# Optimization experiments

Hardware: AMD Instinct MI355X
Metric: run time of the kernel (lower is better)

Reference implementation:

```python
import jax, jax.numpy as jnp
import numpy as np

N_NODES = 50000

def setup_inputs() -> dict:
    key = jax.random.key(0)
    ks = jax.random.split(key, 6)
    x = jax.random.normal(ks[0], (N_NODES, 64), dtype=jnp.float32)
    src = jax.random.randint(ks[1], (800000,), 0, N_NODES, dtype=jnp.int64)
    dst = jax.random.randint(ks[2], (800000,), 0, N_NODES, dtype=jnp.int64)
    W = jax.random.normal(ks[3], (64, 64), dtype=jnp.float32) * (1.0 / np.sqrt(64))
    b = jnp.zeros((64,), dtype=jnp.float32)
    Wr = jax.random.normal(ks[4], (64, 64), dtype=jnp.float32) * (1.0 / np.sqrt(64))
    br = jnp.zeros((64,), dtype=jnp.float32)
    return {"x": x, "src": src, "dst": dst, "W": W, "b": b, "Wr": Wr, "br": br}


def reference(x, src, dst, W, b, Wr, br):
    # DGL GraphConv, norm='both', allow_zero_in_degree=True:
    #   h = D_in^{-1/2} * (A^T (D_out^{-1/2} * x)) @ W + b, degrees clamped to >=1
    n = x.shape[0]
    ones = jnp.ones(src.shape[0], dtype=x.dtype)
    out_deg = jax.ops.segment_sum(ones, src, num_segments=n)  # out-degree of each node
    in_deg = jax.ops.segment_sum(ones, dst, num_segments=n)   # in-degree of each node
    norm_src = jax.lax.rsqrt(jnp.clip(out_deg, 1.0, None))[:, None]  # [N,1]
    norm_dst = jax.lax.rsqrt(jnp.clip(in_deg, 1.0, None))[:, None]   # [N,1]
    x_src = x * norm_src
    # SpMM aggregate: sum messages from src to dst
    agg = jax.ops.segment_sum(x_src[src], dst, num_segments=n)  # [N, in_dim]
    agg = agg * norm_dst
    h = agg @ W + b
    res = x @ Wr + br
    return h + res
```

## Files before the change

### kernel.cpp

```cpp
#include <hip/hip_runtime.h>


#define TILE 4096

typedef __attribute__((ext_vector_type(4))) _Float16 half4;

__global__ __launch_bounds__(256) void bucket_hist_kernel(
    const int* __restrict__ src, const int* __restrict__ dst,
    int* __restrict__ H, int e, int nb) {
    __shared__ int hd[256], hs[256];
    int t = threadIdx.x, blk = blockIdx.x;
    hd[t] = 0; hs[t] = 0;
    __syncthreads();
    int base = blk * TILE;
    #pragma unroll
    for (int s = 0; s < 16; ++s) {
        int j = base + s * 256 + t;
        if (j < e) {
            atomicAdd(&hd[dst[j] >> 8], 1);
            atomicAdd(&hs[src[j] >> 8], 1);
        }
    }
    __syncthreads();
    H[t * nb + blk]            = hd[t];
    H[256 * nb + t * nb + blk] = hs[t];
}

__global__ void partial_kernel(const int* __restrict__ cnt, int* __restrict__ part, int m) {
    __shared__ int sm[256];
    int t = threadIdx.x;
    int base = blockIdx.x * 4096 + t * 16;
    int s = 0;
    if (base + 16 <= m) {
        const int4* p = (const int4*)(cnt + base);
        #pragma unroll
        for (int k = 0; k < 4; ++k) { int4 v = p[k]; s += v.x + v.y + v.z + v.w; }
    } else {
        for (int k = 0; k < 16; ++k) if (base + k < m) s += cnt[base + k];
    }
    sm[t] = s;
    __syncthreads();
    for (int st = 128; st > 0; st >>= 1) {
        if (t < st) sm[t] += sm[t + st];
        __syncthreads();
    }
    if (t == 0) part[blockIdx.x] = sm[0];
}

__global__ void scan_final_kernel(const int* __restrict__ cnt, const int* __restrict__ part,
                                  int* __restrict__ Hoff, int m, int nbs) {
    __shared__ int sm[256], sp[256];
    int t = threadIdx.x;
    int pv = (t < nbs) ? part[t] : 0;
    sp[t] = pv;
    __syncthreads();
    for (int d = 1; d < 256; d <<= 1) {
        int add = (t >= d) ? sp[t - d] : 0;
        __syncthreads();
        sp[t] += add;
        __syncthreads();
    }
    sp[t] -= pv;
    __syncthreads();
    int blkoff = sp[blockIdx.x];

    int base = blockIdx.x * 4096 + t * 16;
    int v[16];
    #pragma unroll
    for (int k = 0; k < 16; ++k) v[k] = (base + k < m) ? cnt[base + k] : 0;
    int s = 0;
    #pragma unroll
    for (int k = 0; k < 16; ++k) { int x = v[k]; v[k] = s; s += x; }
    sm[t] = s;
    __syncthreads();
    for (int d = 1; d < 256; d <<= 1) {
        int add = (t >= d) ? sm[t - d] : 0;
        __syncthreads();
        sm[t] += add;
        __syncthreads();
    }
    int tb = sm[t] - s + blkoff;
    #pragma unroll
    for (int k = 0; k < 16; ++k)
        if (base + k < m) Hoff[base + k] = v[k] + tb;
}

__global__ __launch_bounds__(256) void bucket_scatter_kernel(
    const int* __restrict__ src, const int* __restrict__ dst,
    const int* __restrict__ Hoff,
    int* __restrict__ packed, unsigned char* __restrict__ ksrc2,
    int e, int nb) {
    __shared__ int dcur[256], scur[256];
    int t = threadIdx.x, blk = blockIdx.x;
    dcur[t] = Hoff[t * nb + blk];
    scur[t] = Hoff[256 * nb + t * nb + blk] - e;
    __syncthreads();
    int base = blk * TILE;
    #pragma unroll
    for (int s2 = 0; s2 < 16; ++s2) {
        int j = base + s2 * 256 + t;
        if (j < e) {
            int d = dst[j], sv = src[j];
            int pd = atomicAdd(&dcur[d >> 8], 1);
            packed[pd] = (sv << 8) | (d & 255);
            int ps = atomicAdd(&scur[sv >> 8], 1);
            ksrc2[ps] = (unsigned char)(sv & 255);
        }
    }
}

__global__ __launch_bounds__(256) void csr_outdeg_kernel(
    const int* __restrict__ packed, const unsigned char* __restrict__ ksrc2,
    const int* __restrict__ Hoff,
    int* __restrict__ roff, unsigned short* __restrict__ col,
    const float4* __restrict__ x4, half4* __restrict__ xsh,
    int n, int e, int nb, int nrange) {
    __shared__ int lh[256], sm[256];
    int t = threadIdx.x;
    int r = blockIdx.x;
    if (r < nrange) {
        int beg = Hoff[r * nb];
        int end = (r + 1 < nrange) ? Hoff[(r + 1) * nb] : e;
        lh[t] = 0;
        __syncthreads();
        for (int j = beg + t; j < end; j += 256)
            atomicAdd(&lh[packed[j] & 255], 1);
        __syncthreads();
        int v0 = lh[t];
        sm[t] = v0;
        __syncthreads();
        for (int d = 1; d < 256; d <<= 1) {
            int add = (t >= d) ? sm[t - d] : 0;
            __syncthreads();
            sm[t] += add;
            __syncthreads();
        }
        int excl = sm[t] - v0;
        int v = r * 256 + t;
        if (v < n) roff[v] = beg + excl;
        __syncthreads();
        lh[t] = excl;
        __syncthreads();
        for (int j = beg + t; j < end; j += 256) {
            int p = packed[j];
            int pos = beg + atomicAdd(&lh[p & 255], 1);
            col[pos] = (unsigned short)(p >> 8);
        }
        if (r == 0 && t == 0) roff[n] = e;
    } else {
        r -= nrange;
        lh[t] = 0;
        __syncthreads();
        int beg = Hoff[256 * nb + r * nb] - e;
        int end = (r + 1 < nrange) ? (Hoff[256 * nb + (r + 1) * nb] - e) : e;
        for (int j = beg + t; j < end; j += 256)
            atomicAdd(&lh[ksrc2[j]], 1);
        __syncthreads();
        int base = r * 256;
        for (int i = t; i < 256 * 16; i += 256) {
            int row = i >> 4, g = base + row;
            if (g < n) {
                float s = rsqrtf((float)max(lh[row], 1));
                float4 v = x4[(long)g * 16 + (i & 15)];
                half4 h;
                h.x = (_Float16)(v.x * s);
                h.y = (_Float16)(v.y * s);
                h.z = (_Float16)(v.z * s);
                h.w = (_Float16)(v.w * s);
                xsh[(long)g * 16 + (i & 15)] = h;
            }
        }
    }
}

__global__ __launch_bounds__(256) void gather_kernel(
    const half4* __restrict__ xsh, const unsigned short* __restrict__ col,
    const int* __restrict__ roff,
    float4* __restrict__ agg4, int n) {
    int lane = threadIdx.x & 63;
    int node = (blockIdx.x * 256 + threadIdx.x) >> 6;
    if (node >= n) return;
    node = __builtin_amdgcn_readfirstlane(node);

    int beg = roff[node];
    int end = roff[node + 1];
    int g = lane >> 4;
    int q = lane & 15;

    float4 acc = make_float4(0.f, 0.f, 0.f, 0.f);
    int j = beg;
    for (; j + 16 <= end; j += 16) {
        int s0 = col[j + g];
        int s1 = col[j + 4 + g];
        int s2 = col[j + 8 + g];
        int s3 = col[j + 12 + g];
        half4 v0 = xsh[(long)s0 * 16 + q];
        half4 v1 = xsh[(long)s1 * 16 + q];
        half4 v2 = xsh[(long)s2 * 16 + q];
        half4 v3 = xsh[(long)s3 * 16 + q];
        acc.x += ((float)v0.x + (float)v1.x) + ((float)v2.x + (float)v3.x);
        acc.y += ((float)v0.y + (float)v1.y) + ((float)v2.y + (float)v3.y);
        acc.z += ((float)v0.z + (float)v1.z) + ((float)v2.z + (float)v3.z);
        acc.w += ((float)v0.w + (float)v1.w) + ((float)v2.w + (float)v3.w);
    }
    for (; j + 8 <= end; j += 8) {
        int s0 = col[j + g];
        int s1 = col[j + 4 + g];
        half4 v0 = xsh[(long)s0 * 16 + q];
        half4 v1 = xsh[(long)s1 * 16 + q];
        acc.x += (float)v0.x + (float)v1.x;
        acc.y += (float)v0.y + (float)v1.y;
        acc.z += (float)v0.z + (float)v1.z;
        acc.w += (float)v0.w + (float)v1.w;
    }
    for (; j < end; j += 4) {
        int jj = j + g;
        int s   = (jj < end) ? (int)col[jj] : node;
        float m = (jj < end) ? 1.f : 0.f;
        half4 v = xsh[(long)s * 16 + q];
        acc.x += (float)v.x * m;
        acc.y += (float)v.y * m;
        acc.z += (float)v.z * m;
        acc.w += (float)v.w * m;
    }

    acc.x += __shfl_down(acc.x, 32);
    acc.y += __shfl_down(acc.y, 32);
    acc.z += __shfl_down(acc.z, 32);
    acc.w += __shfl_down(acc.w, 32);
    acc.x += __shfl_down(acc.x, 16);
    acc.y += __shfl_down(acc.y, 16);
    acc.z += __shfl_down(acc.z, 16);
    acc.w += __shfl_down(acc.w, 16);

    float nd = rsqrtf((float)max(end - beg, 1));
    if (lane < 16) {
        acc.x *= nd; acc.y *= nd; acc.z *= nd; acc.w *= nd;
        agg4[(long)node * 16 + q] = acc;
    }
}

#define OR 32
__global__ __launch_bounds__(256) void out_kernel(
    const float4* __restrict__ agg4, const float4* __restrict__ x4,
    const float* __restrict__ W, const float* __restrict__ b,
    const float* __restrict__ Wr, const float* __restrict__ br,
    float* __restrict__ out, int n) {
    __shared__ float4 sA[OR * 16];
    __shared__ float4 sX[OR * 16];
    int t = threadIdx.x;
    int c = t & 63;
    int base = blockIdx.x * OR;

    float4 wA[16], wR[16];
    #pragma unroll
    for (int q = 0; q < 16; ++q) {
        wA[q].x = W[(4 * q + 0) * 64 + c];
        wA[q].y = W[(4 * q + 1) * 64 + c];
        wA[q].z = W[(4 * q + 2) * 64 + c];
        wA[q].w = W[(4 * q + 3) * 64 + c];
        wR[q].x = Wr[(4 * q + 0) * 64 + c];
        wR[q].y = Wr[(4 * q + 1) * 64 + c];
        wR[q].z = Wr[(4 * q + 2) * 64 + c];
        wR[q].w = Wr[(4 * q + 3) * 64 + c];
    }

    #pragma unroll
    for (int i = 0; i < 2; ++i) {
        int qi = t + 256 * i;
        int row = base + (qi >> 4);
        float4 z = make_float4(0.f, 0.f, 0.f, 0.f);
        sA[qi] = (row < n) ? agg4[(long)row * 16 + (qi & 15)] : z;
        sX[qi] = (row < n) ? x4[(long)row * 16 + (qi & 15)] : z;
    }
    __syncthreads();

    int w = t >> 6;
    float bias = b[c] + br[c];
    for (int r = w * 8; r < w * 8 + 8; ++r) {
        float a0 = 0.f, a1 = 0.f, r0 = 0.f, r1 = 0.f;
        #pragma unroll
        for (int q = 0; q < 16; q += 2) {
            float4 av0 = sA[r * 16 + q];
            float4 av1 = sA[r * 16 + q + 1];
            float4 xv0 = sX[r * 16 + q];
            float4 xv1 = sX[r * 16 + q + 1];
            a0 += av0.x * wA[q].x + av0.y * wA[q].y + av0.z * wA[q].z + av0.w * wA[q].w;
            a1 += av1.x * wA[q + 1].x + av1.y * wA[q + 1].y + av1.z * wA[q + 1].z + av1.w * wA[q + 1].w;
            r0 += xv0.x * wR[q].x + xv0.y * wR[q].y + xv0.z * wR[q].z + xv0.w * wR[q].w;
            r1 += xv1.x * wR[q + 1].x + xv1.y * wR[q + 1].y + xv1.z * wR[q + 1].z + xv1.w * wR[q + 1].w;
        }
        int grow = base + r;
        if (grow < n) out[(long)grow * 64 + c] = (a0 + a1) + (r0 + r1) + bias;
    }
}

extern "C" void kernel_launch(void* const* d_in, const int* in_sizes, int n_in,
                              void* d_out, int out_size, void* d_ws, size_t ws_size,
                              hipStream_t stream) {
    const float* x   = (const float*)d_in[0];
    const int*   src = (const int*)d_in[1];
    const int*   dst = (const int*)d_in[2];
    const float* W   = (const float*)d_in[3];
    const float* b   = (const float*)d_in[4];
    const float* Wr  = (const float*)d_in[5];
    const float* br  = (const float*)d_in[6];
    float* out = (float*)d_out;

    const int n = in_sizes[0] / 64;
    const int e = in_sizes[1];
    const int nb = (e + TILE - 1) / TILE;
    const int nrange = (n + 255) / 256;
    const int m = 2 * 256 * nb;
    const int nbs = (m + 4095) / 4096;

    char* p = (char*)d_ws;
    int* H      = (int*)p;  p += (size_t)m * 4;
    int* Hoff   = (int*)p;  p += (size_t)m * 4;
    int* part   = (int*)p;  p += 1024;
    int* packed = (int*)p;  p += (size_t)e * 4;
    int* roff   = (int*)p;  p += (size_t)(n + 1) * 4;
    p = (char*)(((uintptr_t)p + 15) & ~(uintptr_t)15);
    unsigned short* col = (unsigned short*)p;  p += (size_t)e * 2;
    p = (char*)(((uintptr_t)p + 15) & ~(uintptr_t)15);
    half4* xsh  = (half4*)p;  p += (size_t)n * 64 * 2;
    p = (char*)(((uintptr_t)p + 15) & ~(uintptr_t)15);
    float* agg  = (float*)p;  p += (size_t)n * 64 * 4;
    unsigned char* ksrc2 = (unsigned char*)p;

    bucket_hist_kernel<<<nb, 256, 0, stream>>>(src, dst, H, e, nb);

    partial_kernel<<<nbs, 256, 0, stream>>>(H, part, m);
    scan_final_kernel<<<nbs, 256, 0, stream>>>(H, part, Hoff, m, nbs);

    bucket_scatter_kernel<<<nb, 256, 0, stream>>>(src, dst, Hoff, packed, ksrc2, e, nb);

    csr_outdeg_kernel<<<2 * nrange, 256, 0, stream>>>(
        packed, ksrc2, Hoff, roff, col, (const float4*)x, xsh, n, e, nb, nrange);

    gather_kernel<<<(n * 64 + 255) / 256, 256, 0, stream>>>(
        xsh, col, roff, (float4*)agg, n);

    out_kernel<<<(n + OR - 1) / OR, 256, 0, stream>>>(
        (const float4*)agg, (const float4*)x, W, b, Wr, br, out, n);
}
```

Before: 104.6 us.

## Fuse CSR build stages into one cooperative kernel with grid syncs

Merges the histogram, two-pass scan, bucket scatter and CSR/outdegree kernels into a single cooperative launch separated by grid.sync barriers. It also halves the edge tile so there are more histogram/scatter blocks. The goal is to remove several kernel launch gaps and tail drains. The cost is grid-wide barrier overhead, a grid size capped by co-residency, and a histogram twice as large to scan.

```diff
diff --git a/kernel.cpp b/kernel.cpp
--- a/kernel.cpp
+++ b/kernel.cpp
@@ -1,166 +1,164 @@
 #include <hip/hip_runtime.h>
-
-
-#define TILE 4096
+#include <hip/hip_cooperative_groups.h>
+
+namespace cg = cooperative_groups;
+
+
+#define TILE 2048
 
 typedef __attribute__((ext_vector_type(4))) _Float16 half4;
 
-__global__ __launch_bounds__(256) void bucket_hist_kernel(
+__global__ __launch_bounds__(256) void build_kernel(
     const int* __restrict__ src, const int* __restrict__ dst,
-    int* __restrict__ H, int e, int nb) {
-    __shared__ int hd[256], hs[256];
-    int t = threadIdx.x, blk = blockIdx.x;
-    hd[t] = 0; hs[t] = 0;
-    __syncthreads();
-    int base = blk * TILE;
-    #pragma unroll
-    for (int s = 0; s < 16; ++s) {
-        int j = base + s * 256 + t;
-        if (j < e) {
-            atomicAdd(&hd[dst[j] >> 8], 1);
-            atomicAdd(&hs[src[j] >> 8], 1);
-        }
-    }
-    __syncthreads();
-    H[t * nb + blk]            = hd[t];
-    H[256 * nb + t * nb + blk] = hs[t];
-}
-
-__global__ void partial_kernel(const int* __restrict__ cnt, int* __restrict__ part, int m) {
-    __shared__ int sm[256];
-    int t = threadIdx.x;
-    int base = blockIdx.x * 4096 + t * 16;
-    int s = 0;
-    if (base + 16 <= m) {
-        const int4* p = (const int4*)(cnt + base);
-        #pragma unroll
-        for (int k = 0; k < 4; ++k) { int4 v = p[k]; s += v.x + v.y + v.z + v.w; }
-    } else {
-        for (int k = 0; k < 16; ++k) if (base + k < m) s += cnt[base + k];
-    }
-    sm[t] = s;
-    __syncthreads();
-    for (int st = 128; st > 0; st >>= 1) {
-        if (t < st) sm[t] += sm[t + st];
-        __syncthreads();
-    }
-    if (t == 0) part[blockIdx.x] = sm[0];
-}
-
-__global__ void scan_final_kernel(const int* __restrict__ cnt, const int* __restrict__ part,
-                                  int* __restrict__ Hoff, int m, int nbs) {
-    __shared__ int sm[256], sp[256];
-    int t = threadIdx.x;
-    int pv = (t < nbs) ? part[t] : 0;
-    sp[t] = pv;
-    __syncthreads();
-    for (int d = 1; d < 256; d <<= 1) {
-        int add = (t >= d) ? sp[t - d] : 0;
-        __syncthreads();
-        sp[t] += add;
-        __syncthreads();
-    }
-    sp[t] -= pv;
-    __syncthreads();
-    int blkoff = sp[blockIdx.x];
-
-    int base = blockIdx.x * 4096 + t * 16;
-    int v[16];
-    #pragma unroll
-    for (int k = 0; k < 16; ++k) v[k] = (base + k < m) ? cnt[base + k] : 0;
-    int s = 0;
-    #pragma unroll
-    for (int k = 0; k < 16; ++k) { int x = v[k]; v[k] = s; s += x; }
-    sm[t] = s;
-    __syncthreads();
-    for (int d = 1; d < 256; d <<= 1) {
-        int add = (t >= d) ? sm[t - d] : 0;
-        __syncthreads();
-        sm[t] += add;
-        __syncthreads();
-    }
-    int tb = sm[t] - s + blkoff;
-    #pragma unroll
-    for (int k = 0; k < 16; ++k)
-        if (base + k < m) Hoff[base + k] = v[k] + tb;
-}
-
-__global__ __launch_bounds__(256) void bucket_scatter_kernel(
-    const int* __restrict__ src, const int* __restrict__ dst,
-    const int* __restrict__ Hoff,
+    int* __restrict__ H, int* __restrict__ part, int* __restrict__ Hoff,
     int* __restrict__ packed, unsigned char* __restrict__ ksrc2,
-    int e, int nb) {
-    __shared__ int dcur[256], scur[256];
-    int t = threadIdx.x, blk = blockIdx.x;
-    dcur[t] = Hoff[t * nb + blk];
-    scur[t] = Hoff[256 * nb + t * nb + blk] - e;
-    __syncthreads();
-    int base = blk * TILE;
-    #pragma unroll
-    for (int s2 = 0; s2 < 16; ++s2) {
-        int j = base + s2 * 256 + t;
-        if (j < e) {
-            int d = dst[j], sv = src[j];
-            int pd = atomicAdd(&dcur[d >> 8], 1);
-            packed[pd] = (sv << 8) | (d & 255);
-            int ps = atomicAdd(&scur[sv >> 8], 1);
-            ksrc2[ps] = (unsigned char)(sv & 255);
-        }
-    }
-}
-
-__global__ __launch_bounds__(256) void csr_outdeg_kernel(
-    const int* __restrict__ packed, const unsigned char* __restrict__ ksrc2,
-    const int* __restrict__ Hoff,
     int* __restrict__ roff, unsigned short* __restrict__ col,
     const float4* __restrict__ x4, half4* __restrict__ xsh,
-    int n, int e, int nb, int nrange) {
-    __shared__ int lh[256], sm[256];
-    int t = threadIdx.x;
-    int r = blockIdx.x;
-    if (r < nrange) {
+    int n, int e, int nb, int nbs, int nrange) {
+    cg::grid_group grid = cg::this_grid();
+    __shared__ int A[256], B[256];
+    int t = threadIdx.x, blk = blockIdx.x;
+    const int m = 2 * 256 * nb;
+
+    if (blk < nb) {
+        A[t] = 0; B[t] = 0;
+        __syncthreads();
+        int base = blk * TILE;
+        #pragma unroll
+        for (int s = 0; s < 8; ++s) {
+            int j = base + s * 256 + t;
+            if (j < e) {
+                atomicAdd(&A[dst[j] >> 8], 1);
+                atomicAdd(&B[src[j] >> 8], 1);
+            }
+        }
+        __syncthreads();
+        H[t * nb + blk]            = A[t];
+        H[256 * nb + t * nb + blk] = B[t];
+    }
+    grid.sync();
+
+    if (blk < nbs) {
+        int base = blk * 4096 + t * 16;
+        int s = 0;
+        if (base + 16 <= m) {
+            const int4* p4 = (const int4*)(H + base);
+            #pragma unroll
+            for (int k = 0; k < 4; ++k) { int4 v = p4[k]; s += v.x + v.y + v.z + v.w; }
+        } else {
+            for (int k = 0; k < 16; ++k) if (base + k < m) s += H[base + k];
+        }
+        A[t] = s;
+        __syncthreads();
+        for (int st = 128; st > 0; st >>= 1) {
+            if (t < st) A[t] += A[t + st];
+            __syncthreads();
+        }
+        if (t == 0) part[blk] = A[0];
+    }
+    grid.sync();
+
+    if (blk < nbs) {
+        int pv = (t < nbs) ? part[t] : 0;
+        B[t] = pv;
+        __syncthreads();
+        for (int d = 1; d < 256; d <<= 1) {
+            int add = (t >= d) ? B[t - d] : 0;
+            __syncthreads();
+            B[t] += add;
+            __syncthreads();
+        }
+        int ex = B[t] - pv;
+        __syncthreads();
+        B[t] = ex;
+        __syncthreads();
+        int blkoff = B[blk];
+
+        int base = blk * 4096 + t * 16;
+        int v[16];
+        #pragma unroll
+        for (int k = 0; k < 16; ++k) v[k] = (base + k < m) ? H[base + k] : 0;
+        int s = 0;
+        #pragma unroll
+        for (int k = 0; k < 16; ++k) { int x = v[k]; v[k] = s; s += x; }
+        A[t] = s;
+        __syncthreads();
+        for (int d = 1; d < 256; d <<= 1) {
+            int add = (t >= d) ? A[t - d] : 0;
+            __syncthreads();
+            A[t] += add;
+            __syncthreads();
+        }
+        int tb = A[t] - s + blkoff;
+        #pragma unroll
+        for (int k = 0; k < 16; ++k)
+            if (base + k < m) Hoff[base + k] = v[k] + tb;
+    }
+    grid.sync();
+
+    if (blk < nb) {
+        A[t] = Hoff[t * nb + blk];
+        B[t] = Hoff[256 * nb + t * nb + blk] - e;
+        __syncthreads();
+        int base = blk * TILE;
+        #pragma unroll
+        for (int s2 = 0; s2 < 8; ++s2) {
+            int j = base + s2 * 256 + t;
+            if (j < e) {
+                int d = dst[j], sv = src[j];
+                int pd = atomicAdd(&A[d >> 8], 1);
+                packed[pd] = (sv << 8) | (d & 255);
+                int ps = atomicAdd(&B[sv >> 8], 1);
+                ksrc2[ps] = (unsigned char)(sv & 255);
+            }
+        }
+    }
+    grid.sync();
+
+    if (blk < nrange) {
+        int r = blk;
         int beg = Hoff[r * nb];
         int end = (r + 1 < nrange) ? Hoff[(r + 1) * nb] : e;
-        lh[t] = 0;
+        A[t] = 0;
         __syncthreads();
         for (int j = beg + t; j < end; j += 256)
-            atomicAdd(&lh[packed[j] & 255], 1);
-        __syncthreads();
-        int v0 = lh[t];
-        sm[t] = v0;
+            atomicAdd(&A[packed[j] & 255], 1);
+        __syncthreads();
+        int v0 = A[t];
+        B[t] = v0;
         __syncthreads();
         for (int d = 1; d < 256; d <<= 1) {
-            int add = (t >= d) ? sm[t - d] : 0;
-            __syncthreads();
-            sm[t] += add;
-            __syncthreads();
-        }
-        int excl = sm[t] - v0;
+            int add = (t >= d) ? B[t - d] : 0;
+            __syncthreads();
+            B[t] += add;
+            __syncthreads();
+        }
+        int excl = B[t] - v0;
         int v = r * 256 + t;
         if (v < n) roff[v] = beg + excl;
         __syncthreads();
-        lh[t] = excl;
+        A[t] = excl;
         __syncthreads();
         for (int j = beg + t; j < end; j += 256) {
             int p = packed[j];
-            int pos = beg + atomicAdd(&lh[p & 255], 1);
+            int pos = beg + atomicAdd(&A[p & 255], 1);
             col[pos] = (unsigned short)(p >> 8);
         }
         if (r == 0 && t == 0) roff[n] = e;
-    } else {
-        r -= nrange;
-        lh[t] = 0;
+    } else if (blk < 2 * nrange) {
+        int r = blk - nrange;
+        A[t] = 0;
         __syncthreads();
         int beg = Hoff[256 * nb + r * nb] - e;
         int end = (r + 1 < nrange) ? (Hoff[256 * nb + (r + 1) * nb] - e) : e;
         for (int j = beg + t; j < end; j += 256)
-            atomicAdd(&lh[ksrc2[j]], 1);
+            atomicAdd(&A[ksrc2[j]], 1);
         __syncthreads();
         int base = r * 256;
         for (int i = t; i < 256 * 16; i += 256) {
             int row = i >> 4, g = base + row;
             if (g < n) {
-                float s = rsqrtf((float)max(lh[row], 1));
+                float s = rsqrtf((float)max(A[row], 1));
                 float4 v = x4[(long)g * 16 + (i & 15)];
                 half4 h;
                 h.x = (_Float16)(v.x * s);
@@ -307,12 +305,14 @@
     const float* br  = (const float*)d_in[6];
     float* out = (float*)d_out;
 
-    const int n = in_sizes[0] / 64;
-    const int e = in_sizes[1];
-    const int nb = (e + TILE - 1) / TILE;
-    const int nrange = (n + 255) / 256;
-    const int m = 2 * 256 * nb;
-    const int nbs = (m + 4095) / 4096;
+    int n = in_sizes[0] / 64;
+    int e = in_sizes[1];
+    int nb = (e + TILE - 1) / TILE;
+    int nrange = (n + 255) / 256;
+    int m = 2 * 256 * nb;
+    int nbs = (m + 4095) / 4096;
+    int grid = 2 * nrange > nb ? 2 * nrange : nb;
+    if (grid < nbs) grid = nbs;
 
     char* p = (char*)d_ws;
     int* H      = (int*)p;  p += (size_t)m * 4;
@@ -328,15 +328,15 @@
     float* agg  = (float*)p;  p += (size_t)n * 64 * 4;
     unsigned char* ksrc2 = (unsigned char*)p;
 
-    bucket_hist_kernel<<<nb, 256, 0, stream>>>(src, dst, H, e, nb);
-
-    partial_kernel<<<nbs, 256, 0, stream>>>(H, part, m);
-    scan_final_kernel<<<nbs, 256, 0, stream>>>(H, part, Hoff, m, nbs);
-
-    bucket_scatter_kernel<<<nb, 256, 0, stream>>>(src, dst, Hoff, packed, ksrc2, e, nb);
-
-    csr_outdeg_kernel<<<2 * nrange, 256, 0, stream>>>(
-        packed, ksrc2, Hoff, roff, col, (const float4*)x, xsh, n, e, nb, nrange);
+    const float4* x4 = (const float4*)x;
+    void* kargs[] = {
+        (void*)&src, (void*)&dst, (void*)&H, (void*)&part, (void*)&Hoff,
+        (void*)&packed, (void*)&ksrc2, (void*)&roff, (void*)&col,
+        (void*)&x4, (void*)&xsh,
+        (void*)&n, (void*)&e, (void*)&nb, (void*)&nbs, (void*)&nrange
+    };
+    hipLaunchCooperativeKernel((void*)build_kernel, dim3(grid), dim3(256),
+                               kargs, 0, stream);
 
     gather_kernel<<<(n * 64 + 255) / 256, 256, 0, stream>>>(
         xsh, col, roff, (float4*)agg, n);
```

Result: slower. 318.0 us (+203.9%).
